# Performance work log

Measured on AMD Instinct MI355X. Metric: run time of the kernel, lower is better.

Reference implementation:

```python
import jax, jax.numpy as jnp
import numpy as np

DENSITY_FACTOR = 100.0
RAY_SAMPLES = 256
W_RES, H_RES = 320, 240
BS = 4
VOL_D = 128


def setup_inputs() -> dict:
    key = jax.random.key(0)
    k1, k2 = jax.random.split(key)
    vol = jax.random.uniform(k1, (BS, 4, VOL_D, VOL_D, VOL_D), dtype=jnp.float32)
    # per-batch rigid rotation about the y axis (homogeneous 4x4, w component stays 1)
    ang = jax.random.uniform(k2, (BS,), minval=0.0, maxval=2.0 * np.pi, dtype=jnp.float32)
    c, s = jnp.cos(ang), jnp.sin(ang)
    z, o = jnp.zeros_like(c), jnp.ones_like(c)
    tfm = jnp.stack([
        jnp.stack([c, z, s, z], -1),
        jnp.stack([z, o, z, z], -1),
        jnp.stack([-s, z, c, z], -1),
        jnp.stack([z, z, z, o], -1),
    ], axis=1)  # (BS,4,4)
    return {"vol": vol, "tfm": tfm}


def grid_sample_3d(vol, grid):
    """torch.nn.functional.grid_sample (5D, trilinear, zeros padding, align_corners=False).
    vol: (C,D,H,W); grid: (S,Hh,Ww,3) with last dim = (x,y,z) in [-1,1]. -> (C,S,Hh,Ww)"""
    C, D, H, W = vol.shape
    gx, gy, gz = grid[..., 0], grid[..., 1], grid[..., 2]
    # unnormalize, align_corners=False convention
    ix = ((gx + 1.0) * W - 1.0) * 0.5
    iy = ((gy + 1.0) * H - 1.0) * 0.5
    iz = ((gz + 1.0) * D - 1.0) * 0.5
    ix0, iy0, iz0 = jnp.floor(ix), jnp.floor(iy), jnp.floor(iz)
    fx, fy, fz = ix - ix0, iy - iy0, iz - iz0
    out = jnp.zeros((C,) + grid.shape[:-1], vol.dtype)
    for dz in (0, 1):
        for dy in (0, 1):
            for dx in (0, 1):
                xi, yi, zi = ix0 + dx, iy0 + dy, iz0 + dz
                w = ((fx if dx else 1.0 - fx) * (fy if dy else 1.0 - fy)
                     * (fz if dz else 1.0 - fz))
                valid = ((xi >= 0) & (xi < W) & (yi >= 0) & (yi < H)
                         & (zi >= 0) & (zi < D))
                xc = jnp.clip(xi, 0, W - 1).astype(jnp.int32)
                yc = jnp.clip(yi, 0, H - 1).astype(jnp.int32)
                zc = jnp.clip(zi, 0, D - 1).astype(jnp.int32)
                v = vol[:, zc, yc, xc]  # (C,S,Hh,Ww) gather
                out = out + v * (w * valid.astype(vol.dtype))[None]
    return out


def _sample_coords(tfm):
    """Build the transformed sample grid: (BS, S, H, W, 3)."""
    z = jnp.linspace(-1.0, 1.0, RAY_SAMPLES)
    y = jnp.linspace(-1.0, 1.0, H_RES)
    x = jnp.linspace(-1.0, 1.0, W_RES)
    Z, Y, X = jnp.meshgrid(z, y, x, indexing='ij')  # torch.meshgrid default 'ij'
    coords = jnp.stack([X, Y, Z, jnp.ones_like(X)], axis=-1)  # (S,H,W,4) homogenized
    flat = coords.reshape(-1, 4)
    tc = jnp.einsum('bij,nj->bni', tfm, flat).reshape(
        tfm.shape[0], RAY_SAMPLES, H_RES, W_RES, 4)
    return tc[..., :3] / tc[..., 3:4]


def reference(vol, tfm):
    density = vol[:, 3:4]            # (B,1,D,H,W)
    color = vol[:, :3]               # (B,3,D,H,W)
    grid = _sample_coords(tfm.astype(vol.dtype))  # (B,S,H,W,3)
    dens = density * (DENSITY_FACTOR / RAY_SAMPLES)
    ds = jax.vmap(grid_sample_3d)(dens, grid)        # (B,1,S,H,W)
    transmission = jnp.cumprod(1.0 - ds, axis=2)     # sequential scan over rays
    weight = ds * transmission                       # (B,1,S,H,W)
    w_sum = jnp.sum(weight, axis=2)                  # (B,1,H,W)
    cs = jax.vmap(grid_sample_3d)(color, grid)       # (B,3,S,H,W)
    render = jnp.sum(weight * cs, axis=2) / (w_sum + 1e-6)  # (B,3,H,W)
    alpha = 1.0 - transmission[:, :, -1]             # == 1 - prod(1-ds, axis=2)
    return render * alpha
```

## Files before the change

### kernel.cpp

```cpp
#include <hip/hip_runtime.h>

namespace {

constexpr int W_RES = 320, H_RES = 240, BS = 4, VD = 128, NS = 256;
constexpr float DENS_SCALE = 100.0f / 256.0f / 255.0f;
constexpr float TAU = 5e-4f;
constexpr long long VOX = (long long)VD * VD * VD;

__global__ void transpose_k(const float* __restrict__ vol, uint4* __restrict__ out) {
    long long tid = (long long)blockIdx.x * blockDim.x + threadIdx.x;
    const long long npair = (long long)BS * VOX / 2;
    if (tid >= npair) return;
    int b = (int)(tid / (VOX / 2));
    long long r = (tid - (long long)b * (VOX / 2)) * 2;
    int x = (int)(r & (VD - 1));
    bool last = (x == VD - 2);
    const float* vb = vol + (long long)b * 4 * VOX + r;
    float2 R = *(const float2*)(vb);
    float2 G = *(const float2*)(vb + VOX);
    float2 Bl = *(const float2*)(vb + 2 * VOX);
    float2 Dn = *(const float2*)(vb + 3 * VOX);
    float R2 = last ? 0.0f : vb[2];
    float G2 = last ? 0.0f : vb[VOX + 2];
    float B2 = last ? 0.0f : vb[2 * VOX + 2];
    float D2 = last ? 0.0f : vb[3 * VOX + 2];
    auto pk = [](float r_, float g_, float bl_, float d_) -> unsigned {
        unsigned ur = (unsigned)(r_ * 255.0f + 0.5f);
        unsigned ug = (unsigned)(g_ * 255.0f + 0.5f);
        unsigned ub = (unsigned)(bl_ * 255.0f + 0.5f);
        unsigned ud = (unsigned)(d_ * 255.0f + 0.5f);
        return ur | (ug << 8) | (ub << 16) | (ud << 24);
    };
    unsigned p0 = pk(R.x, G.x, Bl.x, Dn.x);
    unsigned p1 = pk(R.y, G.y, Bl.y, Dn.y);
    unsigned p2 = pk(R2, G2, B2, D2);
    uint4 o;
    o.x = p0; o.y = p1;
    o.z = p1; o.w = p2;
    out[tid] = o;
}

struct St {
    uint2 p[4];
    float wzy[4];
    float wlo, whi;
};

struct Coord {
    int x0, y0, z0;
    float fx, fy, fz;
    bool fast;
};

__device__ __forceinline__ Coord mkc(float ix, float iy, float iz) {
    Coord c;
    float f;
    f = floorf(ix); c.fx = ix - f; c.x0 = (int)f;
    f = floorf(iy); c.fy = iy - f; c.y0 = (int)f;
    f = floorf(iz); c.fz = iz - f; c.z0 = (int)f;
    c.fast = ((unsigned)c.x0 < 128u) & ((unsigned)c.y0 < 127u) & ((unsigned)c.z0 < 127u);
    return c;
}

__device__ __forceinline__ void stage_fast(const uint2* __restrict__ vb,
                                           const Coord& c, St& st) {
    const uint2* r0 = vb + ((c.z0 * VD + c.y0) * VD + c.x0);
    const uint2* r1 = r0 + VD * VD;
    st.p[0] = r0[0];
    st.p[1] = r0[VD];
    st.p[2] = r1[0];
    st.p[3] = r1[VD];
    st.wlo = 1.0f - c.fx;
    st.whi = c.fx;
    float wy0 = 1.0f - c.fy, wy1 = c.fy;
    float wz0 = 1.0f - c.fz, wz1 = c.fz;
    st.wzy[0] = wz0 * wy0; st.wzy[1] = wz0 * wy1;
    st.wzy[2] = wz1 * wy0; st.wzy[3] = wz1 * wy1;
}

__device__ __forceinline__ void stage_safe(const uint2* __restrict__ vb,
                                           const Coord& c, St& st) {
    int x0 = c.x0, y0 = c.y0, z0 = c.z0;
    bool in01x = ((unsigned)x0 < 128u);
    bool ism1 = (x0 == -1);
    st.wlo = in01x ? (1.0f - c.fx) : (ism1 ? c.fx : 0.0f);
    st.whi = in01x ? c.fx : 0.0f;
    int bx = min(max(x0, 0), 127);

    float my0 = ((unsigned)y0 < 128u) ? 1.0f : 0.0f;
    float my1 = ((unsigned)(y0 + 1) < 128u) ? 1.0f : 0.0f;
    float mz0 = ((unsigned)z0 < 128u) ? 1.0f : 0.0f;
    float mz1 = ((unsigned)(z0 + 1) < 128u) ? 1.0f : 0.0f;
    int yc0 = min(max(y0, 0), 127), yc1 = min(max(y0 + 1, 0), 127);
    int zc0 = min(max(z0, 0), 127), zc1 = min(max(z0 + 1, 0), 127);

    st.p[0] = vb[(zc0 * VD + yc0) * VD + bx];
    st.p[1] = vb[(zc0 * VD + yc1) * VD + bx];
    st.p[2] = vb[(zc1 * VD + yc0) * VD + bx];
    st.p[3] = vb[(zc1 * VD + yc1) * VD + bx];

    float wy0 = (1.0f - c.fy) * my0, wy1 = c.fy * my1;
    float wz0 = (1.0f - c.fz) * mz0, wz1 = c.fz * mz1;
    st.wzy[0] = wz0 * wy0; st.wzy[1] = wz0 * wy1;
    st.wzy[2] = wz1 * wy0; st.wzy[3] = wz1 * wy1;
}

__device__ __forceinline__ void consume(const St& st, float& T, float& wsum,
                                        float& aR, float& aG, float& aB) {
    float ar = 0, ag = 0, ab = 0, ad = 0;
#pragma unroll
    for (int i = 0; i < 4; ++i) {
        unsigned lo = st.p[i].x, hi = st.p[i].y;
        float wl = st.wzy[i] * st.wlo;
        float wh = st.wzy[i] * st.whi;
        ar = fmaf(wl, (float)(lo & 255u), ar);
        ag = fmaf(wl, (float)((lo >> 8) & 255u), ag);
        ab = fmaf(wl, (float)((lo >> 16) & 255u), ab);
        ad = fmaf(wl, (float)(lo >> 24), ad);
        ar = fmaf(wh, (float)(hi & 255u), ar);
        ag = fmaf(wh, (float)((hi >> 8) & 255u), ag);
        ab = fmaf(wh, (float)((hi >> 16) & 255u), ab);
        ad = fmaf(wh, (float)(hi >> 24), ad);
    }
    float dsv = ad * DENS_SCALE;
    T *= (1.0f - dsv);
    float wgt = dsv * T;
    wsum += wgt;
    aR = fmaf(wgt, ar, aR);
    aG = fmaf(wgt, ag, aG);
    aB = fmaf(wgt, ab, aB);
}

__global__ void __launch_bounds__(256) raycast_k(const uint2* __restrict__ vol,
                                                 const float* __restrict__ tfm,
                                                 float* __restrict__ out) {
    constexpr int NPIX = W_RES * H_RES;
    int lane = threadIdx.x & 63;
    int wave = threadIdx.x >> 6;
    int bx = blockIdx.x % (W_RES / 16);
    int rest = blockIdx.x / (W_RES / 16);
    int by = rest % (H_RES / 16);
    int b = rest / (H_RES / 16);
    int x = bx * 16 + (lane & 15);
    int y = by * 16 + wave * 4 + (lane >> 4);

    float X = -1.0f + 2.0f * x / (float)(W_RES - 1);
    float Y = -1.0f + 2.0f * y / (float)(H_RES - 1);
    const float dZ = 2.0f / (float)(NS - 1);

    const float* M = tfm + b * 16;
    float bxc = M[0] * X + M[1] * Y + M[3];
    float byc = M[4] * X + M[5] * Y + M[7];
    float bzc = M[8] * X + M[9] * Y + M[11];
    float bwc = M[12] * X + M[13] * Y + M[15];
    float m02 = M[2], m12 = M[6], m22 = M[10], m32 = M[14];

    const uint2* vb = vol + (long long)b * VOX;

    bool w1 = (fabsf(bwc - 1.0f) < 1e-6f) && (fabsf(m32) < 1e-6f);
    float lo = 0.0f, hi = (float)(NS - 1);
    if (w1) {
        const float LIM = 1.0078125f + 1e-5f;
        auto clipAxis = [&](float bb, float mm) {
            float A = bb - mm;
            float Bq = mm * dZ;
            if (fabsf(Bq) < 1e-9f) {
                if (fabsf(A) > LIM) { lo = 1.0f; hi = 0.0f; }
            } else {
                float s1 = (-LIM - A) / Bq, s2 = (LIM - A) / Bq;
                lo = fmaxf(lo, fminf(s1, s2));
                hi = fminf(hi, fmaxf(s1, s2));
            }
        };
        clipAxis(bxc, m02);
        clipAxis(byc, m12);
        clipAxis(bzc, m22);
    }
    int s_start = max(0, (int)ceilf(lo - 1e-3f));
    int s_end = min(NS - 1, (int)floorf(hi + 1e-3f));

    int wsv = s_start, wev = s_end;
#pragma unroll
    for (int off = 1; off < 64; off <<= 1) {
        wsv = min(wsv, __shfl_xor(wsv, off));
        wev = max(wev, __shfl_xor(wev, off));
    }

    auto coords = [&](int s, float& ix, float& iy, float& iz) {
        float Z = fmaf((float)s, dZ, -1.0f);
        float gx = fmaf(m02, Z, bxc);
        float gy = fmaf(m12, Z, byc);
        float gz = fmaf(m22, Z, bzc);
        if (!w1) {
            float iw = 1.0f / fmaf(m32, Z, bwc);
            gx *= iw; gy *= iw; gz *= iw;
        }
        ix = fmaf(gx, 64.0f, 63.5f);
        iy = fmaf(gy, 64.0f, 63.5f);
        iz = fmaf(gz, 64.0f, 63.5f);
    };

    float T = 1.0f, wsum = 0.0f, aR = 0.0f, aG = 0.0f, aB = 0.0f;
    St S0, S1, S2;

    for (int s = wsv; s <= wev; s += 3) {
        bool alive = (T >= TAU);
        bool g0 = (s >= s_start) & (s <= s_end) & alive;
        bool g1 = (s + 1 >= s_start) & (s + 1 <= s_end) & alive;
        bool g2 = (s + 2 >= s_start) & (s + 2 <= s_end) & alive;
        Coord c0, c1, c2;
        float ix, iy, iz;
        if (g0) { coords(s, ix, iy, iz); c0 = mkc(ix, iy, iz); }
        if (g1) { coords(s + 1, ix, iy, iz); c1 = mkc(ix, iy, iz); }
        if (g2) { coords(s + 2, ix, iy, iz); c2 = mkc(ix, iy, iz); }
        bool fastAll = __all((g0 ? c0.fast : true) & (g1 ? c1.fast : true) &
                             (g2 ? c2.fast : true));
        if (fastAll) {
            if (g0) stage_fast(vb, c0, S0);
            if (g1) stage_fast(vb, c1, S1);
            if (g2) stage_fast(vb, c2, S2);
        } else {
            if (g0) stage_safe(vb, c0, S0);
            if (g1) stage_safe(vb, c1, S1);
            if (g2) stage_safe(vb, c2, S2);
        }
        __builtin_amdgcn_sched_barrier(0);
        if (g0) consume(S0, T, wsum, aR, aG, aB);
        if (g1 & (T >= TAU)) consume(S1, T, wsum, aR, aG, aB);
        if (g2 & (T >= TAU)) consume(S2, T, wsum, aR, aG, aB);
        if (!__any((T >= TAU) & (s + 3 <= s_end))) break;
    }

    float scale = (1.0f - T) / (wsum + 1e-6f) * (1.0f / 255.0f);
    int po = y * W_RES + x;
    float* ob = out + (long long)b * 3 * NPIX;
    ob[po] = aR * scale;
    ob[po + NPIX] = aG * scale;
    ob[po + 2 * NPIX] = aB * scale;
}

}

extern "C" void kernel_launch(void* const* d_in, const int* in_sizes, int n_in,
                              void* d_out, int out_size, void* d_ws, size_t ws_size,
                              hipStream_t stream) {
    const float* vol = (const float*)d_in[0];
    const float* tfm = (const float*)d_in[1];
    float* out = (float*)d_out;

    uint4* v8 = (uint4*)d_ws;
    (void)ws_size; (void)in_sizes; (void)n_in; (void)out_size;

    const long long npair = (long long)BS * VOX / 2;
    transpose_k<<<(int)((npair + 255) / 256), 256, 0, stream>>>(vol, v8);

    const int nblk = (W_RES / 16) * (H_RES / 16) * BS;
    raycast_k<<<nblk, 256, 0, stream>>>((const uint2*)v8, tfm, out);
}
```

Measured before the change: 148.5 us.

## Split each ray into four depth segments and combine partial composites

The ray-marching kernel now divides each wave's sample range into K_SEG=4 segments, each handled by a separate block, and writes partial color/weight sums and segment transmittance to workspace. A new combine kernel composes the segments front-to-back into the final render. This raises parallelism from 1200 blocks to 4800 so more of the GPU is occupied and the long serial march is shortened. In exchange, early termination can no longer skip later segments, so total sampling work may grow, and there is an extra launch plus workspace traffic.

Measured after the change: 261.4 us. +76.1%, slower.

```diff
diff --git a/kernel.cpp b/kernel.cpp
--- a/kernel.cpp
+++ b/kernel.cpp
@@ -3,9 +3,14 @@
 namespace {
 
 constexpr int W_RES = 320, H_RES = 240, BS = 4, VD = 128, NS = 256;
+constexpr int NPIX = W_RES * H_RES;
+constexpr int K_SEG = 4;
 constexpr float DENS_SCALE = 100.0f / 256.0f / 255.0f;
 constexpr float TAU = 5e-4f;
 constexpr long long VOX = (long long)VD * VD * VD;
+
+constexpr size_t VOL_BYTES = (size_t)BS * VOX * 8;
+constexpr size_t SEGA_BYTES = (size_t)K_SEG * BS * NPIX * 16;
 
 __global__ void transpose_k(const float* __restrict__ vol, uint4* __restrict__ out) {
     long long tid = (long long)blockIdx.x * blockDim.x + threadIdx.x;
@@ -133,14 +138,14 @@
 
 __global__ void __launch_bounds__(256) raycast_k(const uint2* __restrict__ vol,
                                                  const float* __restrict__ tfm,
-                                                 float* __restrict__ out) {
-    constexpr int NPIX = W_RES * H_RES;
+                                                 float4* __restrict__ segA,
+                                                 float* __restrict__ segT) {
     int lane = threadIdx.x & 63;
     int wave = threadIdx.x >> 6;
-    int bx = blockIdx.x % (W_RES / 16);
-    int rest = blockIdx.x / (W_RES / 16);
-    int by = rest % (H_RES / 16);
-    int b = rest / (H_RES / 16);
+    int bx = blockIdx.x;
+    int by = blockIdx.y;
+    int k = blockIdx.z & (K_SEG - 1);
+    int b = blockIdx.z >> 2;
     int x = bx * 16 + (lane & 15);
     int y = by * 16 + wave * 4 + (lane >> 4);
 
@@ -179,12 +184,25 @@
     int s_start = max(0, (int)ceilf(lo - 1e-3f));
     int s_end = min(NS - 1, (int)floorf(hi + 1e-3f));
 
-    int wsv = s_start, wev = s_end;
+    int rs = (s_start <= s_end) ? s_start : 0x7fffffff;
+    int re = (s_start <= s_end) ? s_end : -0x7fffffff;
 #pragma unroll
     for (int off = 1; off < 64; off <<= 1) {
-        wsv = min(wsv, __shfl_xor(wsv, off));
-        wev = max(wev, __shfl_xor(wev, off));
-    }
+        rs = min(rs, __shfl_xor(rs, off));
+        re = max(re, __shfl_xor(re, off));
+    }
+
+    float T = 1.0f, wsum = 0.0f, aR = 0.0f, aG = 0.0f, aB = 0.0f;
+
+    int segLo = 1, segHi = 0;
+    if (rs <= re) {
+        int L = re - rs + 1;
+        int slen = (L + K_SEG - 1) / K_SEG;
+        segLo = rs + k * slen;
+        segHi = min(re, segLo + slen - 1);
+    }
+
+    int se = min(s_end, segHi);
 
     auto coords = [&](int s, float& ix, float& iy, float& iz) {
         float Z = fmaf((float)s, dZ, -1.0f);
@@ -200,14 +218,12 @@
         iz = fmaf(gz, 64.0f, 63.5f);
     };
 
-    float T = 1.0f, wsum = 0.0f, aR = 0.0f, aG = 0.0f, aB = 0.0f;
     St S0, S1, S2;
-
-    for (int s = wsv; s <= wev; s += 3) {
+    for (int s = segLo; s <= segHi; s += 3) {
         bool alive = (T >= TAU);
-        bool g0 = (s >= s_start) & (s <= s_end) & alive;
-        bool g1 = (s + 1 >= s_start) & (s + 1 <= s_end) & alive;
-        bool g2 = (s + 2 >= s_start) & (s + 2 <= s_end) & alive;
+        bool g0 = (s >= s_start) & (s <= se) & alive;
+        bool g1 = (s + 1 >= s_start) & (s + 1 <= se) & alive;
+        bool g2 = (s + 2 >= s_start) & (s + 2 <= se) & alive;
         Coord c0, c1, c2;
         float ix, iy, iz;
         if (g0) { coords(s, ix, iy, iz); c0 = mkc(ix, iy, iz); }
@@ -228,15 +244,38 @@
         if (g0) consume(S0, T, wsum, aR, aG, aB);
         if (g1 & (T >= TAU)) consume(S1, T, wsum, aR, aG, aB);
         if (g2 & (T >= TAU)) consume(S2, T, wsum, aR, aG, aB);
-        if (!__any((T >= TAU) & (s + 3 <= s_end))) break;
-    }
-
-    float scale = (1.0f - T) / (wsum + 1e-6f) * (1.0f / 255.0f);
-    int po = y * W_RES + x;
+        if (!__any((T >= TAU) & (s + 3 <= segHi))) break;
+    }
+
+    long long sidx = ((long long)k * BS + b) * NPIX + y * W_RES + x;
+    segA[sidx] = make_float4(aR, aG, aB, wsum);
+    segT[sidx] = T;
+}
+
+__global__ void combine_k(const float4* __restrict__ segA,
+                          const float* __restrict__ segT,
+                          float* __restrict__ out) {
+    int tid = blockIdx.x * blockDim.x + threadIdx.x;
+    if (tid >= BS * NPIX) return;
+    float aR = 0, aG = 0, aB = 0, ws = 0, Tg = 1.0f;
+#pragma unroll
+    for (int k = 0; k < K_SEG; ++k) {
+        long long idx = (long long)k * BS * NPIX + tid;
+        float4 a = segA[idx];
+        float t = segT[idx];
+        aR = fmaf(Tg, a.x, aR);
+        aG = fmaf(Tg, a.y, aG);
+        aB = fmaf(Tg, a.z, aB);
+        ws = fmaf(Tg, a.w, ws);
+        Tg *= t;
+    }
+    float scale = (1.0f - Tg) / (ws + 1e-6f) * (1.0f / 255.0f);
+    int b = tid / NPIX;
+    int pix = tid - b * NPIX;
     float* ob = out + (long long)b * 3 * NPIX;
-    ob[po] = aR * scale;
-    ob[po + NPIX] = aG * scale;
-    ob[po + 2 * NPIX] = aB * scale;
+    ob[pix] = aR * scale;
+    ob[pix + NPIX] = aG * scale;
+    ob[pix + 2 * NPIX] = aB * scale;
 }
 
 }
@@ -248,12 +287,17 @@
     const float* tfm = (const float*)d_in[1];
     float* out = (float*)d_out;
 
-    uint4* v8 = (uint4*)d_ws;
+    unsigned char* ws = (unsigned char*)d_ws;
+    uint4* v8 = (uint4*)ws;
+    float4* segA = (float4*)(ws + VOL_BYTES);
+    float* segT = (float*)(ws + VOL_BYTES + SEGA_BYTES);
     (void)ws_size; (void)in_sizes; (void)n_in; (void)out_size;
 
     const long long npair = (long long)BS * VOX / 2;
     transpose_k<<<(int)((npair + 255) / 256), 256, 0, stream>>>(vol, v8);
 
-    const int nblk = (W_RES / 16) * (H_RES / 16) * BS;
-    raycast_k<<<nblk, 256, 0, stream>>>((const uint2*)v8, tfm, out);
-}
+    dim3 grid(W_RES / 16, H_RES / 16, BS * K_SEG);
+    raycast_k<<<grid, 256, 0, stream>>>((const uint2*)v8, tfm, segA, segT);
+
+    combine_k<<<(BS * NPIX + 255) / 256, 256, 0, stream>>>(segA, segT, out);
+}
```

## Split ray marching into head pass plus two parallel tail segments with combine

Applied to the files above, without the earlier changes.

Ray marching is split into three kernels. The first marches the first 64 samples per ray and saves a checkpoint. The second runs only for rays still above the transmittance cutoff and marches the rest of the ray as two independent halves, each starting from T=1. A combine kernel then composites the segments front to back. The aim is more parallelism and less serial per-ray latency for long-surviving rays, at the cost of extra launches, checkpoint traffic, fp16-packed wsum/T precision, and wasted samples in the second half for rays that would have terminated early.

After: 208.0 us. +40.1%, slower.

```diff
diff --git a/kernel.cpp b/kernel.cpp
--- a/kernel.cpp
+++ b/kernel.cpp
@@ -1,11 +1,29 @@
 #include <hip/hip_runtime.h>
+#include <hip/hip_fp16.h>
 
 namespace {
 
 constexpr int W_RES = 320, H_RES = 240, BS = 4, VD = 128, NS = 256;
+constexpr int NPIX = W_RES * H_RES;
+constexpr int ACAP = 64;
 constexpr float DENS_SCALE = 100.0f / 256.0f / 255.0f;
 constexpr float TAU = 5e-4f;
 constexpr long long VOX = (long long)VD * VD * VD;
+
+constexpr size_t VOL_BYTES = (size_t)BS * VOX * 8;
+constexpr size_t CKPT_BYTES = (size_t)BS * NPIX * 16;
+
+__device__ __forceinline__ unsigned h2u(__half2 h) {
+    unsigned u; __builtin_memcpy(&u, &h, 4); return u;
+}
+__device__ __forceinline__ float pack_wT(float ws, float T) {
+    return __builtin_bit_cast(float, h2u(__floats2half2_rn(ws, T)));
+}
+__device__ __forceinline__ void unpack_wT(float p, float& ws, float& T) {
+    unsigned u = __builtin_bit_cast(unsigned, p);
+    __half2 h; __builtin_memcpy(&h, &u, 4);
+    ws = __half2float(__low2half(h)); T = __half2float(__high2half(h));
+}
 
 __global__ void transpose_k(const float* __restrict__ vol, uint4* __restrict__ out) {
     long long tid = (long long)blockIdx.x * blockDim.x + threadIdx.x;
@@ -131,35 +149,25 @@
     aB = fmaf(wgt, ab, aB);
 }
 
-__global__ void __launch_bounds__(256) raycast_k(const uint2* __restrict__ vol,
-                                                 const float* __restrict__ tfm,
-                                                 float* __restrict__ out) {
-    constexpr int NPIX = W_RES * H_RES;
-    int lane = threadIdx.x & 63;
-    int wave = threadIdx.x >> 6;
-    int bx = blockIdx.x % (W_RES / 16);
-    int rest = blockIdx.x / (W_RES / 16);
-    int by = rest % (H_RES / 16);
-    int b = rest / (H_RES / 16);
-    int x = bx * 16 + (lane & 15);
-    int y = by * 16 + wave * 4 + (lane >> 4);
-
+struct Ray {
+    float bxc, byc, bzc, bwc, m02, m12, m22, m32;
+    bool w1;
+    int s_start, s_end;
+};
+
+__device__ __forceinline__ Ray make_ray(const float* __restrict__ M, int x, int y) {
+    Ray r;
     float X = -1.0f + 2.0f * x / (float)(W_RES - 1);
     float Y = -1.0f + 2.0f * y / (float)(H_RES - 1);
     const float dZ = 2.0f / (float)(NS - 1);
-
-    const float* M = tfm + b * 16;
-    float bxc = M[0] * X + M[1] * Y + M[3];
-    float byc = M[4] * X + M[5] * Y + M[7];
-    float bzc = M[8] * X + M[9] * Y + M[11];
-    float bwc = M[12] * X + M[13] * Y + M[15];
-    float m02 = M[2], m12 = M[6], m22 = M[10], m32 = M[14];
-
-    const uint2* vb = vol + (long long)b * VOX;
-
-    bool w1 = (fabsf(bwc - 1.0f) < 1e-6f) && (fabsf(m32) < 1e-6f);
+    r.bxc = M[0] * X + M[1] * Y + M[3];
+    r.byc = M[4] * X + M[5] * Y + M[7];
+    r.bzc = M[8] * X + M[9] * Y + M[11];
+    r.bwc = M[12] * X + M[13] * Y + M[15];
+    r.m02 = M[2]; r.m12 = M[6]; r.m22 = M[10]; r.m32 = M[14];
+    r.w1 = (fabsf(r.bwc - 1.0f) < 1e-6f) && (fabsf(r.m32) < 1e-6f);
     float lo = 0.0f, hi = (float)(NS - 1);
-    if (w1) {
+    if (r.w1) {
         const float LIM = 1.0078125f + 1e-5f;
         auto clipAxis = [&](float bb, float mm) {
             float A = bb - mm;
@@ -172,47 +180,55 @@
                 hi = fminf(hi, fmaxf(s1, s2));
             }
         };
-        clipAxis(bxc, m02);
-        clipAxis(byc, m12);
-        clipAxis(bzc, m22);
-    }
-    int s_start = max(0, (int)ceilf(lo - 1e-3f));
-    int s_end = min(NS - 1, (int)floorf(hi + 1e-3f));
-
-    int wsv = s_start, wev = s_end;
+        clipAxis(r.bxc, r.m02);
+        clipAxis(r.byc, r.m12);
+        clipAxis(r.bzc, r.m22);
+    }
+    r.s_start = max(0, (int)ceilf(lo - 1e-3f));
+    r.s_end = min(NS - 1, (int)floorf(hi + 1e-3f));
+    return r;
+}
+
+__device__ __forceinline__ void ray_coords(const Ray& r, int s,
+                                           float& ix, float& iy, float& iz) {
+    const float dZ = 2.0f / (float)(NS - 1);
+    float Z = fmaf((float)s, dZ, -1.0f);
+    float gx = fmaf(r.m02, Z, r.bxc);
+    float gy = fmaf(r.m12, Z, r.byc);
+    float gz = fmaf(r.m22, Z, r.bzc);
+    if (!r.w1) {
+        float iw = 1.0f / fmaf(r.m32, Z, r.bwc);
+        gx *= iw; gy *= iw; gz *= iw;
+    }
+    ix = fmaf(gx, 64.0f, 63.5f);
+    iy = fmaf(gy, 64.0f, 63.5f);
+    iz = fmaf(gz, 64.0f, 63.5f);
+}
+
+__device__ __forceinline__ void march(const uint2* __restrict__ vb, const Ray& r,
+                                      int sLo, int sHi, float& T, float& wsum,
+                                      float& aR, float& aG, float& aB) {
+    bool ok = (sLo <= sHi);
+    int lo_l = ok ? sLo : 0x7fffffff;
+    int hi_l = ok ? sHi : (-0x7fffffff - 1);
 #pragma unroll
     for (int off = 1; off < 64; off <<= 1) {
-        wsv = min(wsv, __shfl_xor(wsv, off));
-        wev = max(wev, __shfl_xor(wev, off));
-    }
-
-    auto coords = [&](int s, float& ix, float& iy, float& iz) {
-        float Z = fmaf((float)s, dZ, -1.0f);
-        float gx = fmaf(m02, Z, bxc);
-        float gy = fmaf(m12, Z, byc);
-        float gz = fmaf(m22, Z, bzc);
-        if (!w1) {
-            float iw = 1.0f / fmaf(m32, Z, bwc);
-            gx *= iw; gy *= iw; gz *= iw;
-        }
-        ix = fmaf(gx, 64.0f, 63.5f);
-        iy = fmaf(gy, 64.0f, 63.5f);
-        iz = fmaf(gz, 64.0f, 63.5f);
-    };
-
-    float T = 1.0f, wsum = 0.0f, aR = 0.0f, aG = 0.0f, aB = 0.0f;
+        lo_l = min(lo_l, __shfl_xor(lo_l, off));
+        hi_l = max(hi_l, __shfl_xor(hi_l, off));
+    }
+    if (lo_l > hi_l) return;
+
     St S0, S1, S2;
-
-    for (int s = wsv; s <= wev; s += 3) {
-        bool alive = (T >= TAU);
-        bool g0 = (s >= s_start) & (s <= s_end) & alive;
-        bool g1 = (s + 1 >= s_start) & (s + 1 <= s_end) & alive;
-        bool g2 = (s + 2 >= s_start) & (s + 2 <= s_end) & alive;
+    for (int s = lo_l; s <= hi_l; s += 3) {
+        bool alive = ok & (T >= TAU);
+        bool g0 = (s >= sLo) & (s <= sHi) & alive;
+        bool g1 = (s + 1 >= sLo) & (s + 1 <= sHi) & alive;
+        bool g2 = (s + 2 >= sLo) & (s + 2 <= sHi) & alive;
         Coord c0, c1, c2;
         float ix, iy, iz;
-        if (g0) { coords(s, ix, iy, iz); c0 = mkc(ix, iy, iz); }
-        if (g1) { coords(s + 1, ix, iy, iz); c1 = mkc(ix, iy, iz); }
-        if (g2) { coords(s + 2, ix, iy, iz); c2 = mkc(ix, iy, iz); }
+        if (g0) { ray_coords(r, s, ix, iy, iz); c0 = mkc(ix, iy, iz); }
+        if (g1) { ray_coords(r, s + 1, ix, iy, iz); c1 = mkc(ix, iy, iz); }
+        if (g2) { ray_coords(r, s + 2, ix, iy, iz); c2 = mkc(ix, iy, iz); }
         bool fastAll = __all((g0 ? c0.fast : true) & (g1 ? c1.fast : true) &
                              (g2 ? c2.fast : true));
         if (fastAll) {
@@ -228,15 +244,96 @@
         if (g0) consume(S0, T, wsum, aR, aG, aB);
         if (g1 & (T >= TAU)) consume(S1, T, wsum, aR, aG, aB);
         if (g2 & (T >= TAU)) consume(S2, T, wsum, aR, aG, aB);
-        if (!__any((T >= TAU) & (s + 3 <= s_end))) break;
-    }
-
-    float scale = (1.0f - T) / (wsum + 1e-6f) * (1.0f / 255.0f);
-    int po = y * W_RES + x;
+        if (!__any(ok & (T >= TAU) & (s + 3 <= sHi))) break;
+    }
+}
+
+__global__ void __launch_bounds__(256) raycastA_k(const uint2* __restrict__ vol,
+                                                  const float* __restrict__ tfm,
+                                                  float4* __restrict__ ckpt) {
+    int lane = threadIdx.x & 63;
+    int wave = threadIdx.x >> 6;
+    int b = blockIdx.z;
+    int x = blockIdx.x * 16 + (lane & 15);
+    int y = blockIdx.y * 16 + wave * 4 + (lane >> 4);
+
+    Ray r = make_ray(tfm + b * 16, x, y);
+    const uint2* vb = vol + (long long)b * VOX;
+
+    float T = 1.0f, wsum = 0.0f, aR = 0.0f, aG = 0.0f, aB = 0.0f;
+    int sLo = r.s_start;
+    int sHi = min(r.s_end, r.s_start + ACAP - 1);
+    if (r.s_start > r.s_end) { sLo = 1; sHi = 0; }
+    march(vb, r, sLo, sHi, T, wsum, aR, aG, aB);
+
+    ckpt[(long long)b * NPIX + y * W_RES + x] =
+        make_float4(aR, aG, aB, pack_wT(wsum, T));
+}
+
+__global__ void __launch_bounds__(256) raycastB_k(const uint2* __restrict__ vol,
+                                                  const float* __restrict__ tfm,
+                                                  const float4* __restrict__ ckpt,
+                                                  float4* __restrict__ seg) {
+    int lane = threadIdx.x & 63;
+    int wave = threadIdx.x >> 6;
+    int k = blockIdx.z & 1;
+    int b = blockIdx.z >> 1;
+    int x = blockIdx.x * 16 + (lane & 15);
+    int y = blockIdx.y * 16 + wave * 4 + (lane >> 4);
+
+    Ray r = make_ray(tfm + b * 16, x, y);
+    const uint2* vb = vol + (long long)b * VOX;
+    long long pidx = (long long)b * NPIX + y * W_RES + x;
+
+    float T = 1.0f, wsum = 0.0f, aR = 0.0f, aG = 0.0f, aB = 0.0f;
+
+    int sLo = 1, sHi = 0;
+    if (r.s_start <= r.s_end) {
+        int base = r.s_start + ACAP;
+        if (base <= r.s_end) {
+            float wsA, TA;
+            unpack_wT(ckpt[pidx].w, wsA, TA);
+            if (TA >= TAU) {
+                int remLen = r.s_end - base + 1;
+                int L = (remLen + 1) >> 1;
+                sLo = base + k * L;
+                sHi = min(r.s_end, sLo + L - 1);
+                if (sLo > r.s_end) { sLo = 1; sHi = 0; }
+            }
+        }
+    }
+    march(vb, r, sLo, sHi, T, wsum, aR, aG, aB);
+
+    seg[(long long)k * BS * NPIX + pidx] = make_float4(aR, aG, aB, pack_wT(wsum, T));
+}
+
+__global__ void combine_k(const float4* __restrict__ ckpt,
+                          const float4* __restrict__ seg,
+                          float* __restrict__ out) {
+    int tid = blockIdx.x * blockDim.x + threadIdx.x;
+    if (tid >= BS * NPIX) return;
+    float4 a0 = ckpt[tid];
+    float ws, Tg;
+    unpack_wT(a0.w, ws, Tg);
+    float aR = a0.x, aG = a0.y, aB = a0.z;
+#pragma unroll
+    for (int k = 0; k < 2; ++k) {
+        float4 a = seg[(long long)k * BS * NPIX + tid];
+        float wsk, Tk;
+        unpack_wT(a.w, wsk, Tk);
+        aR = fmaf(Tg, a.x, aR);
+        aG = fmaf(Tg, a.y, aG);
+        aB = fmaf(Tg, a.z, aB);
+        ws = fmaf(Tg, wsk, ws);
+        Tg *= Tk;
+    }
+    float scale = (1.0f - Tg) / (ws + 1e-6f) * (1.0f / 255.0f);
+    int b = tid / NPIX;
+    int pix = tid - b * NPIX;
     float* ob = out + (long long)b * 3 * NPIX;
-    ob[po] = aR * scale;
-    ob[po + NPIX] = aG * scale;
-    ob[po + 2 * NPIX] = aB * scale;
+    ob[pix] = aR * scale;
+    ob[pix + NPIX] = aG * scale;
+    ob[pix + 2 * NPIX] = aB * scale;
 }
 
 }
@@ -248,12 +345,20 @@
     const float* tfm = (const float*)d_in[1];
     float* out = (float*)d_out;
 
-    uint4* v8 = (uint4*)d_ws;
+    unsigned char* ws = (unsigned char*)d_ws;
+    uint4* v8 = (uint4*)ws;
+    float4* ckpt = (float4*)(ws + VOL_BYTES);
+    float4* seg = (float4*)(ws + VOL_BYTES + CKPT_BYTES);
     (void)ws_size; (void)in_sizes; (void)n_in; (void)out_size;
 
     const long long npair = (long long)BS * VOX / 2;
     transpose_k<<<(int)((npair + 255) / 256), 256, 0, stream>>>(vol, v8);
 
-    const int nblk = (W_RES / 16) * (H_RES / 16) * BS;
-    raycast_k<<<nblk, 256, 0, stream>>>((const uint2*)v8, tfm, out);
-}
+    dim3 gA(W_RES / 16, H_RES / 16, BS);
+    raycastA_k<<<gA, 256, 0, stream>>>((const uint2*)v8, tfm, ckpt);
+
+    dim3 gB(W_RES / 16, H_RES / 16, BS * 2);
+    raycastB_k<<<gB, 256, 0, stream>>>((const uint2*)v8, tfm, ckpt, seg);
+
+    combine_k<<<(BS * NPIX + 255) / 256, 256, 0, stream>>>(ckpt, seg, out);
+}
```
